# Optimization experiments

Measured on AMD Instinct MI355X. Metric: run time of the kernel, lower is better.

## Reference

```python
import jax, jax.numpy as jnp
import numpy as np

K = 5            # dimW
PARAM_SIGMA = 0.08
LAMBDA_V = 2.0
C_MID = 192


def _conv5(x, w, b):
    # standard 5x5 SAME conv (the linear 'm' term of INRF)
    y = jax.lax.conv_general_dilated(x, w, (1, 1), 'SAME',
                                     dimension_numbers=('NCHW', 'OIHW', 'NCHW'))
    return y + b[None, :, None, None]


def _inrf(x, m_w, m_b, w_w):
    """INRF layer: out = (m * x) - lambda * sum_y w(y) sigma(x(y) - (g*x)(center)).
    dimG=1 so the Gaussian g*x is the identity (center pixel). The radiometric
    nonlinearity sigma is a saturating tanh with slope 1/paramSigma.
    """
    B, C, H, W = x.shape
    # windowed gather: [B, C*K*K, H, W], channel-major / spatial-minor ordering
    patches = jax.lax.conv_general_dilated_patches(x, (K, K), (1, 1), 'SAME')
    patches = patches.reshape(B, C, K * K, H, W)
    s = jnp.tanh((patches - x[:, :, None]) / PARAM_SIGMA)   # [B,C,KK,H,W]
    wterm = jnp.einsum('bckhw,ock->bohw', s, w_w)           # [B,Cout,H,W]
    return _conv5(x, m_w, m_b) - LAMBDA_V * wterm


def _maxpool2(x):
    return jax.lax.reduce_window(x, -jnp.inf, jax.lax.max,
                                 (1, 1, 2, 2), (1, 1, 2, 2), 'VALID')


def _avgpool8(x):
    s = jax.lax.reduce_window(x, 0.0, jax.lax.add,
                              (1, 1, 8, 8), (1, 1, 8, 8), 'VALID')
    return s / 64.0


def setup_inputs() -> dict:
    key = jax.random.key(0)
    ks = jax.random.split(key, 11)
    B = 64
    f32 = jnp.float32
    return {
        'x':    jax.random.normal(ks[0], (B, 3, 32, 32), f32),
        'm1_w': jax.random.normal(ks[1], (C_MID, 3, K, K), f32) * 0.05,
        'm1_b': jnp.zeros((C_MID,), f32),
        'w1_w': jax.random.normal(ks[2], (C_MID, 3, K * K), f32) * 0.05,
        'm2_w': jax.random.normal(ks[3], (C_MID, C_MID, K, K), f32) * 0.02,
        'm2_b': jnp.zeros((C_MID,), f32),
        'w2_w': jax.random.normal(ks[4], (C_MID, C_MID, K * K), f32) * 0.02,
        'm3_w': jax.random.normal(ks[5], (C_MID, C_MID, K, K), f32) * 0.02,
        'm3_b': jnp.zeros((C_MID,), f32),
        'w3_w': jax.random.normal(ks[6], (C_MID, C_MID, K * K), f32) * 0.02,
        'fc_w': jax.random.normal(ks[7], (10, C_MID), f32) * 0.05,
        'fc_b': jnp.zeros((10,), f32),
    }


def reference(x, m1_w, m1_b, w1_w, m2_w, m2_b, w2_w,
              m3_w, m3_b, w3_w, fc_w, fc_b):
    # dropout layers run in eval mode (identity); dp2d1 has p=0.0 anyway
    x00 = _maxpool2(_inrf(x, m1_w, m1_b, w1_w))      # [B,192,16,16]
    x01 = _inrf(x00, m2_w, m2_b, w2_w)               # [B,192,16,16]
    x03 = _maxpool2(x01)                             # [B,192,8,8]
    x04 = _inrf(x03, m3_w, m3_b, w3_w)               # [B,192,8,8]
    x05 = _avgpool8(x04)                             # [B,192,1,1]
    feat = x05.reshape(-1, C_MID)
    logits = feat @ fc_w.T + fc_b                    # [B,10]
    return (logits, x00, x01)
```

## Files before the change

### kernel.cpp

```cpp
#include <hip/hip_runtime.h>
#include <math.h>

#define COUT 192
#define NF 12

typedef __bf16 bf16_8 __attribute__((ext_vector_type(8)));
typedef float  f32x4  __attribute__((ext_vector_type(4)));

__device__ __forceinline__ float fast_tanh125(float d) {
    float e = __builtin_amdgcn_exp2f(d * 36.06737602222409f);
    return 1.0f - 2.0f * __builtin_amdgcn_rcpf(e + 1.0f);
}

__device__ __forceinline__ void gl_lds16(const void* gptr, void* lptr) {
    auto g = (const __attribute__((address_space(1))) unsigned int*)gptr;
    auto l = (__attribute__((address_space(3))) unsigned int*)lptr;
    __builtin_amdgcn_global_load_lds(g, l, 16, 0, 0);
}

__global__ void prep_all(const float* __restrict__ m1_w, const float* __restrict__ w1_w,
                         const float* __restrict__ m2_w, const float* __restrict__ w2_w,
                         const float* __restrict__ m3_w, const float* __restrict__ w3_w,
                         __bf16* __restrict__ Bp1, __bf16* __restrict__ Bp2,
                         __bf16* __restrict__ Bp3) {
    int idx = blockIdx.x * 256 + threadIdx.x;
    const int N1 = 3 * 2 * NF * 64, N2 = 192 * 2 * NF * 64;
    const float *mw, *ww; __bf16* Bp; int CIN, li;
    if (idx < N1)           { mw = m1_w; ww = w1_w; Bp = Bp1; CIN = 3;   li = idx; }
    else if (idx < N1 + N2) { mw = m2_w; ww = w2_w; Bp = Bp2; CIN = 192; li = idx - N1; }
    else if (idx < N1 + 2 * N2) { mw = m3_w; ww = w3_w; Bp = Bp3; CIN = 192; li = idx - N1 - N2; }
    else return;
    int lane = li & 63;
    int nf = (li >> 6) % NF;
    int cc = li / (NF * 64);
    int t = cc & 1, c = cc >> 1;
    int n = nf * 16 + (lane & 15);
    int k0 = (lane >> 4) * 8;
    bf16_8 v;
    #pragma unroll
    for (int e = 0; e < 8; ++e) {
        int k = k0 + e;
        float val = 0.f;
        if (k < 25) {
            val = (t == 0) ? mw[((size_t)n * CIN + c) * 25 + k]
                           : -2.0f * ww[((size_t)n * CIN + c) * 25 + k];
        }
        v[e] = (__bf16)val;
    }
    *(bf16_8*)(Bp + (size_t)li * 8) = v;
}

__global__ __launch_bounds__(256, 3) void inrf1_mfma(
    const float* __restrict__ x, const __bf16* __restrict__ Bp,
    const float* __restrict__ bias, float* __restrict__ x00)
{
    __shared__ float win[3][6][36];
    __shared__ float hp[192][33];

    const int b  = blockIdx.x >> 4;
    const int h0 = (blockIdx.x & 15) * 2;
    const int tid = threadIdx.x;
    const int wv = tid >> 6, lane = tid & 63;
    const int hl = wv >> 1, half = wv & 1;
    const int mcol = lane & 15, q = lane >> 4;
    const int wpos = half * 16 + mcol;

    for (int i = tid; i < 3 * 6 * 36; i += 256) {
        int c = i / 216, r = (i / 36) % 6, cc = i % 36;
        int gr = h0 + r - 2, gc = cc - 2;
        float v = 0.f;
        if (gr >= 0 && gr < 32 && gc >= 0 && gc < 32)
            v = x[((size_t)(b * 3 + c) * 32 + gr) * 32 + gc];
        win[c][r][cc] = v;
    }
    __syncthreads();

    int offs[8];
    #pragma unroll
    for (int e = 0; e < 8; ++e) {
        int k = q * 8 + e;
        int kk = (k < 25) ? k : 0;
        offs[e] = (hl + kk / 5) * 36 + wpos + (kk % 5);
    }
    const int cen_off = (hl + 2) * 36 + wpos + 2;

    f32x4 acc[NF];
    #pragma unroll
    for (int j = 0; j < NF; ++j) acc[j] = (f32x4){0.f, 0.f, 0.f, 0.f};

    const float* winf = &win[0][0][0];
    for (int c = 0; c < 3; ++c) {
        const float* wf = winf + c * 216;
        float cen = wf[cen_off];
        bf16_8 av, as_;
        #pragma unroll
        for (int e = 0; e < 8; ++e) {
            float v = wf[offs[e]];
            av[e] = (__bf16)v;
            as_[e] = (__bf16)fast_tanh125(v - cen);
        }
        const bf16_8* b0 = (const bf16_8*)Bp + ((size_t)(c * 2 + 0) * NF) * 64 + lane;
        const bf16_8* b1 = b0 + NF * 64;
        #pragma unroll
        for (int j = 0; j < NF; ++j)
            acc[j] = __builtin_amdgcn_mfma_f32_16x16x32_bf16(av, b0[j * 64], acc[j], 0, 0, 0);
        #pragma unroll
        for (int j = 0; j < NF; ++j)
            acc[j] = __builtin_amdgcn_mfma_f32_16x16x32_bf16(as_, b1[j * 64], acc[j], 0, 0, 0);
    }

    #pragma unroll
    for (int j = 0; j < NF; ++j) {
        int n = j * 16 + mcol;
        hp[n][hl * 16 + half * 8 + q * 2 + 0] = fmaxf(acc[j][0], acc[j][1]);
        hp[n][hl * 16 + half * 8 + q * 2 + 1] = fmaxf(acc[j][2], acc[j][3]);
    }
    __syncthreads();

    const int hpout = h0 >> 1;
    for (int i = tid; i < 192 * 16; i += 256) {
        int n = i >> 4, wp = i & 15;
        float v = fmaxf(hp[n][wp], hp[n][16 + wp]) + bias[n];
        x00[((size_t)(b * COUT + n) * 16 + hpout) * 16 + wp] = v;
    }
}

__global__ __launch_bounds__(512, 2) void inrf2_mfma(
    const float* __restrict__ xin, const __bf16* __restrict__ Bp,
    float* __restrict__ out0, float* __restrict__ part)
{
    constexpr int CPS = 48;
    __shared__ __align__(16) __bf16 Bs[3][24 * 64 * 8];
    __shared__ float win[3][420];

    const int b  = blockIdx.x >> 2;
    const int ks = blockIdx.x & 3;
    const int c0 = ks * CPS;
    const int tid = threadIdx.x;
    const int wv = tid >> 6, lane = tid & 63;
    const int mg = wv & 3, nh = wv >> 2;
    const int wp = lane & 15, q = lane >> 4;

    int offs[8];
    #pragma unroll
    for (int e = 0; e < 8; ++e) {
        int k = q * 8 + e;
        int kk = (k < 25) ? k : 0;
        offs[e] = (kk / 5) * 21 + (kk % 5);
    }

    const int r0_ = tid / 20, c0_ = tid % 20;
    const int w0i = r0_ * 21 + c0_;
    const bool in0 = tid < 400;
    const bool ok0 = in0 && (r0_ >= 2 && r0_ < 18 && c0_ >= 2 && c0_ < 18);
    const float* xb = xin + (size_t)b * COUT * 256;

    f32x4 acc[4][6];
    #pragma unroll
    for (int m = 0; m < 4; ++m)
        #pragma unroll
        for (int j = 0; j < 6; ++j) acc[m][j] = (f32x4){0.f, 0.f, 0.f, 0.f};

#define BUILD_A(SLOT, AV, AS)                                              \
    {                                                                      \
        const float* wc = win[(SLOT)];                                     \
        _Pragma("unroll")                                                  \
        for (int m = 0; m < 4; ++m) {                                      \
            const int base = (mg * 4 + m) * 21 + wp;                       \
            float cen = wc[base + 44];                                     \
            _Pragma("unroll")                                              \
            for (int e = 0; e < 8; ++e) {                                  \
                float v = wc[base + offs[e]];                              \
                (AV)[m][e] = (__bf16)v;                                    \
                (AS)[m][e] = (__bf16)fast_tanh125(v - cen);                \
            }                                                              \
        }                                                                  \
    }

    #pragma unroll
    for (int rr = 0; rr < 2; ++rr) {
        const int c = c0 + rr;
        float v0 = 0.f;
        if (ok0) v0 = xb[(size_t)c * 256 + (r0_ - 2) * 16 + (c0_ - 2)];
        const __bf16* gB = Bp + (size_t)c * 12288 + wv * 1536 + lane * 8;
        #pragma unroll
        for (int i = 0; i < 3; ++i)
            gl_lds16(gB + i * 512, &Bs[rr][wv * 1536 + i * 512]);
        if (in0) win[rr][w0i] = v0;
    }
    __syncthreads();

    bf16_8 av[4], as_[4];
    BUILD_A(0, av, as_);

    #pragma unroll 3
    for (int r = 0; r < CPS; ++r) {
        const int sl_cur = r % 3;
        const int sl_n1  = (r + 1) % 3;
        const int sl_n2  = (r + 2) % 3;
        const bool do2 = (r + 2) < CPS;
        const bool do1 = (r + 1) < CPS;

        float v0 = 0.f;
        if (do2) {
            const int c = c0 + r + 2;
            if (ok0) v0 = xb[(size_t)c * 256 + (r0_ - 2) * 16 + (c0_ - 2)];
            const __bf16* gB = Bp + (size_t)c * 12288 + wv * 1536 + lane * 8;
            #pragma unroll
            for (int i = 0; i < 3; ++i)
                gl_lds16(gB + i * 512, &Bs[sl_n2][wv * 1536 + i * 512]);
        }

        bf16_8 avN[4], asN[4];
        if (do1) BUILD_A(sl_n1, avN, asN);

        const bf16_8* Bf = (const bf16_8*)(Bs[sl_cur]) + lane;
        #pragma unroll
        for (int j = 0; j < 6; ++j) {
            bf16_8 fm = Bf[(nh * 6 + j) * 64];
            bf16_8 fs = Bf[(12 + nh * 6 + j) * 64];
            #pragma unroll
            for (int m = 0; m < 4; ++m) {
                acc[m][j] = __builtin_amdgcn_mfma_f32_16x16x32_bf16(av[m],  fm, acc[m][j], 0, 0, 0);
                acc[m][j] = __builtin_amdgcn_mfma_f32_16x16x32_bf16(as_[m], fs, acc[m][j], 0, 0, 0);
            }
        }

        if (do2 && in0) win[sl_n2][w0i] = v0;

        if (do1) {
            #pragma unroll
            for (int m = 0; m < 4; ++m) { av[m] = avN[m]; as_[m] = asN[m]; }
        }
        __syncthreads();
    }
#undef BUILD_A

    float* outp = (ks == 0) ? out0 : (part + (size_t)(ks - 1) * 3145728);
    #pragma unroll
    for (int j = 0; j < 6; ++j) {
        int n = (nh * 6 + j) * 16 + wp;
        #pragma unroll
        for (int m = 0; m < 4; ++m) {
            int h = mg * 4 + m;
            *(f32x4*)&outp[((size_t)(b * COUT + n)) * 256 + h * 16 + q * 4] = acc[m][j];
        }
    }
}

__global__ __launch_bounds__(512) void finish2(
    float* __restrict__ x01, const float* __restrict__ part,
    const float* __restrict__ bias, __bf16* __restrict__ An)
{
    __shared__ float xbuf[8][256];
    const int b  = blockIdx.x / 24;
    const int cg = blockIdx.x % 24;
    const int tid = threadIdx.x;
    const int wv = tid >> 6, lane = tid & 63;
    const int ch = cg * 8 + wv;

    float* p0 = x01 + ((size_t)b * COUT + ch) * 256;
    const float* pp = part + ((size_t)b * COUT + ch) * 256;
    const float bv = bias[ch];
    #pragma unroll
    for (int i = 0; i < 4; ++i) {
        int idx = lane + 64 * i;
        float s = ((p0[idx] + pp[idx]) + pp[idx + 3145728]) + pp[idx + 2 * 3145728] + bv;
        xbuf[wv][idx] = s;
        p0[idx] = s;
    }
    __syncthreads();

    const int ph = lane >> 3, pw = lane & 7;
    const int i0 = ph * 32 + pw * 2;
    float x8 = fmaxf(fmaxf(xbuf[wv][i0], xbuf[wv][i0 + 1]),
                     fmaxf(xbuf[wv][i0 + 16], xbuf[wv][i0 + 17]));

    float myT = 0.f, myW = 0.f;
    #pragma unroll
    for (int k = 0; k < 25; ++k) {
        const int dy = k / 5 - 2, dx = k % 5 - 2;
        const bool valid = (ph + dy >= 0) && (ph + dy < 8) && (pw + dx >= 0) && (pw + dx < 8);
        float nb = __shfl(x8, (lane + dy * 8 + dx) & 63);
        nb = valid ? nb : 0.f;
        float tS = fast_tanh125(nb - x8);
        float wS = nb;
        #pragma unroll
        for (int off = 1; off < 64; off <<= 1) {
            tS += __shfl_xor(tS, off);
            wS += __shfl_xor(wS, off);
        }
        if (lane == k) { myT = tS; myW = wS; }
    }

    const int mt = b >> 4;
    if (lane < 25) {
        const int k = lane;
        const int la = (k >> 3) * 16 + (b & 15);
        const int e = k & 7;
        const int ccW = ch * 2, ccT = ch * 2 + 1;
        An[((size_t)(ccW * 4 + mt) * 64 + la) * 8 + e] = (__bf16)(myW * 0.015625f);
        An[((size_t)(ccT * 4 + mt) * 64 + la) * 8 + e] = (__bf16)(myT * 0.015625f);
    } else if (lane < 32) {
        const int la = 3 * 16 + (b & 15);
        const int e = lane & 7;
        const int ccW = ch * 2, ccT = ch * 2 + 1;
        An[((size_t)(ccW * 4 + mt) * 64 + la) * 8 + e] = (__bf16)0.f;
        An[((size_t)(ccT * 4 + mt) * 64 + la) * 8 + e] = (__bf16)0.f;
    }
}

__global__ __launch_bounds__(512) void gemm3p(
    const __bf16* __restrict__ An, const __bf16* __restrict__ Bp,
    float* __restrict__ part)
{
    const int ks = blockIdx.x;
    const int tid = threadIdx.x;
    const int wv = tid >> 6, lane = tid & 63;
    const int mt = wv & 3, nh = wv >> 2;

    f32x4 acc[6];
    #pragma unroll
    for (int j = 0; j < 6; ++j) acc[j] = (f32x4){0.f, 0.f, 0.f, 0.f};

    for (int i = 0; i < 4; ++i) {
        const int cc = ks * 4 + i;
        bf16_8 a = *(const bf16_8*)(An + ((size_t)(cc * 4 + mt) * 64 + lane) * 8);
        #pragma unroll
        for (int j = 0; j < 6; ++j) {
            bf16_8 bw = *(const bf16_8*)(Bp + ((size_t)(cc * NF + nh * 6 + j) * 64 + lane) * 8);
            acc[j] = __builtin_amdgcn_mfma_f32_16x16x32_bf16(a, bw, acc[j], 0, 0, 0);
        }
    }
    #pragma unroll
    for (int j = 0; j < 6; ++j) {
        int n = (nh * 6 + j) * 16 + (lane & 15);
        *(f32x4*)(part + ((size_t)ks * COUT + n) * 64 + mt * 16 + (lane >> 4) * 4) = acc[j];
    }
}

__global__ __launch_bounds__(256) void logitsk(
    const float* __restrict__ part, const float* __restrict__ m3_b,
    const float* __restrict__ fc_w, const float* __restrict__ fc_b,
    float* __restrict__ logits)
{
    __shared__ float feat[COUT];
    const int b = blockIdx.x;
    const int t = threadIdx.x;
    if (t < COUT) {
        float s = 0.f;
        for (int ks = 0; ks < 96; ++ks) s += part[((size_t)ks * COUT + t) * 64 + b];
        feat[t] = s + m3_b[t];
    }
    __syncthreads();
    if (t < 10) {
        float s = fc_b[t];
        #pragma unroll 8
        for (int c = 0; c < COUT; ++c) s = fmaf(fc_w[t * COUT + c], feat[c], s);
        logits[(size_t)b * 10 + t] = s;
    }
}

extern "C" void kernel_launch(void* const* d_in, const int* in_sizes, int n_in,
                              void* d_out, int out_size, void* d_ws, size_t ws_size,
                              hipStream_t stream) {
    const float* x    = (const float*)d_in[0];
    const float* m1_w = (const float*)d_in[1];
    const float* m1_b = (const float*)d_in[2];
    const float* w1_w = (const float*)d_in[3];
    const float* m2_w = (const float*)d_in[4];
    const float* m2_b = (const float*)d_in[5];
    const float* w2_w = (const float*)d_in[6];
    const float* m3_w = (const float*)d_in[7];
    const float* m3_b = (const float*)d_in[8];
    const float* w3_w = (const float*)d_in[9];
    const float* fc_w = (const float*)d_in[10];
    const float* fc_b = (const float*)d_in[11];

    float* out = (float*)d_out;
    float* ws  = (float*)d_ws;

    float* logits = out;
    float* x00 = out + 640;
    float* x01 = out + 640 + 3145728;

    __bf16* Bp1  = (__bf16*)(ws);
    __bf16* Bp2  = (__bf16*)(ws + 18432);
    __bf16* Bp3  = (__bf16*)(ws + 1198080);
    __bf16* An   = (__bf16*)(ws + 2377728);
    float*  part2 = ws + 2770944;
    float*  part3 = ws + 2770944;

    prep_all<<<2322, 256, 0, stream>>>(m1_w, w1_w, m2_w, w2_w, m3_w, w3_w, Bp1, Bp2, Bp3);

    inrf1_mfma<<<64 * 16, 256, 0, stream>>>(x, Bp1, m1_b, x00);
    inrf2_mfma<<<64 * 4, 512, 0, stream>>>(x00, Bp2, x01, part2);
    finish2<<<64 * 24, 512, 0, stream>>>(x01, part2, m2_b, An);
    gemm3p<<<96, 512, 0, stream>>>(An, Bp3, part3);
    logitsk<<<64, 256, 0, stream>>>(part3, m3_b, fc_w, fc_b, logits);
}
```

Measured before the change: 223.8 us.

## Load input slab via async global_load_lds and use vmcnt-based barriers

Replaces the padded 20x21 register-staged input window with a raw 16x16 slab loaded directly into LDS with global_load_lds, using precomputed per-element offsets that point to a zero pad for out-of-bounds taps. Full __syncthreads is replaced with inline s_waitcnt vmcnt(N)+s_barrier so that the two-stage-ahead loads stay in flight across iterations. The A-fragment build (tanh) moves from being prefetched one step ahead to the current iteration, which lowers register pressure but puts that work on the critical path before the MFMAs. The hand-written waitcnt assembly relies on the compiler's instruction ordering and counts.

```diff
diff --git a/kernel.cpp b/kernel.cpp
--- a/kernel.cpp
+++ b/kernel.cpp
@@ -17,6 +17,12 @@
     auto l = (__attribute__((address_space(3))) unsigned int*)lptr;
     __builtin_amdgcn_global_load_lds(g, l, 16, 0, 0);
 }
+
+#define BAR_VM4()  asm volatile("s_waitcnt vmcnt(4)\n\ts_barrier" ::: "memory")
+#define BAR_VM3()  asm volatile("s_waitcnt vmcnt(3)\n\ts_barrier" ::: "memory")
+#define BAR_VM0()  asm volatile("s_waitcnt vmcnt(0)\n\ts_barrier" ::: "memory")
+#define BAR_VM4L() asm volatile("s_waitcnt vmcnt(4) lgkmcnt(0)\n\ts_barrier" ::: "memory")
+#define BAR_VM3L() asm volatile("s_waitcnt vmcnt(3) lgkmcnt(0)\n\ts_barrier" ::: "memory")
 
 __global__ void prep_all(const float* __restrict__ m1_w, const float* __restrict__ w1_w,
                          const float* __restrict__ m2_w, const float* __restrict__ w2_w,
@@ -131,7 +137,7 @@
 {
     constexpr int CPS = 48;
     __shared__ __align__(16) __bf16 Bs[3][24 * 64 * 8];
-    __shared__ float win[3][420];
+    __shared__ __align__(16) float slab[3][260];
 
     const int b  = blockIdx.x >> 2;
     const int ks = blockIdx.x & 3;
@@ -141,18 +147,22 @@
     const int mg = wv & 3, nh = wv >> 2;
     const int wp = lane & 15, q = lane >> 4;
 
-    int offs[8];
-    #pragma unroll
-    for (int e = 0; e < 8; ++e) {
-        int k = q * 8 + e;
-        int kk = (k < 25) ? k : 0;
-        offs[e] = (kk / 5) * 21 + (kk % 5);
-    }
-
-    const int r0_ = tid / 20, c0_ = tid % 20;
-    const int w0i = r0_ * 21 + c0_;
-    const bool in0 = tid < 400;
-    const bool ok0 = in0 && (r0_ >= 2 && r0_ < 18 && c0_ >= 2 && c0_ < 18);
+    int aoff[4][8];
+    int cen_off[4];
+    #pragma unroll
+    for (int m = 0; m < 4; ++m) {
+        const int crow = mg * 4 + m;
+        cen_off[m] = crow * 16 + wp;
+        #pragma unroll
+        for (int e = 0; e < 8; ++e) {
+            int kk = q * 8 + e;
+            int dy = kk / 5 - 2, dx = kk % 5 - 2;
+            int rr = crow + dy, cc2 = wp + dx;
+            bool ok = (kk < 25) && (rr >= 0) && (rr < 16) && (cc2 >= 0) && (cc2 < 16);
+            aoff[m][e] = ok ? (rr * 16 + cc2) : 256;
+        }
+    }
+
     const float* xb = xin + (size_t)b * COUT * 256;
 
     f32x4 acc[4][6];
@@ -163,56 +173,50 @@
 
 #define BUILD_A(SLOT, AV, AS)                                              \
     {                                                                      \
-        const float* wc = win[(SLOT)];                                     \
+        const float* sb = slab[(SLOT)];                                    \
         _Pragma("unroll")                                                  \
         for (int m = 0; m < 4; ++m) {                                      \
-            const int base = (mg * 4 + m) * 21 + wp;                       \
-            float cen = wc[base + 44];                                     \
+            float cen = sb[cen_off[m]];                                    \
             _Pragma("unroll")                                              \
             for (int e = 0; e < 8; ++e) {                                  \
-                float v = wc[base + offs[e]];                              \
+                float v = sb[aoff[m][e]];                                  \
                 (AV)[m][e] = (__bf16)v;                                    \
                 (AS)[m][e] = (__bf16)fast_tanh125(v - cen);                \
             }                                                              \
         }                                                                  \
     }
 
+    if (tid < 12) slab[tid >> 2][256 + (tid & 3)] = 0.f;
+
     #pragma unroll
     for (int rr = 0; rr < 2; ++rr) {
         const int c = c0 + rr;
-        float v0 = 0.f;
-        if (ok0) v0 = xb[(size_t)c * 256 + (r0_ - 2) * 16 + (c0_ - 2)];
+        if (wv == 0) gl_lds16(xb + (size_t)c * 256 + lane * 4, &slab[rr][0]);
         const __bf16* gB = Bp + (size_t)c * 12288 + wv * 1536 + lane * 8;
         #pragma unroll
         for (int i = 0; i < 3; ++i)
             gl_lds16(gB + i * 512, &Bs[rr][wv * 1536 + i * 512]);
-        if (in0) win[rr][w0i] = v0;
-    }
-    __syncthreads();
+    }
+    if (wv == 0) { BAR_VM4L(); } else { BAR_VM3L(); }
 
     bf16_8 av[4], as_[4];
-    BUILD_A(0, av, as_);
 
     #pragma unroll 3
     for (int r = 0; r < CPS; ++r) {
         const int sl_cur = r % 3;
-        const int sl_n1  = (r + 1) % 3;
         const int sl_n2  = (r + 2) % 3;
         const bool do2 = (r + 2) < CPS;
-        const bool do1 = (r + 1) < CPS;
-
-        float v0 = 0.f;
+
         if (do2) {
             const int c = c0 + r + 2;
-            if (ok0) v0 = xb[(size_t)c * 256 + (r0_ - 2) * 16 + (c0_ - 2)];
+            if (wv == 0) gl_lds16(xb + (size_t)c * 256 + lane * 4, &slab[sl_n2][0]);
             const __bf16* gB = Bp + (size_t)c * 12288 + wv * 1536 + lane * 8;
             #pragma unroll
             for (int i = 0; i < 3; ++i)
                 gl_lds16(gB + i * 512, &Bs[sl_n2][wv * 1536 + i * 512]);
         }
 
-        bf16_8 avN[4], asN[4];
-        if (do1) BUILD_A(sl_n1, avN, asN);
+        BUILD_A(sl_cur, av, as_);
 
         const bf16_8* Bf = (const bf16_8*)(Bs[sl_cur]) + lane;
         #pragma unroll
@@ -226,13 +230,11 @@
             }
         }
 
-        if (do2 && in0) win[sl_n2][w0i] = v0;
-
-        if (do1) {
-            #pragma unroll
-            for (int m = 0; m < 4; ++m) { av[m] = avN[m]; as_[m] = asN[m]; }
-        }
-        __syncthreads();
+        if (do2) {
+            if (wv == 0) { BAR_VM4(); } else { BAR_VM3(); }
+        } else {
+            BAR_VM0();
+        }
     }
 #undef BUILD_A
 
```

After: 230.2 us. 2.9% more time.
